# Kernel tuning notes

Measured on AMD Instinct MI355X. Metric: run time of the kernel, lower is better.

Reference implementation:

```python
import jax, jax.numpy as jnp
import numpy as np

B, S, D, H = 2, 2048, 1024, 16
DK = D // H
DFF = 4 * D
EPS = 1e-6


def layer_norm(x, gamma, beta):
    mu = jnp.mean(x, axis=-1, keepdims=True)
    var = jnp.mean(jnp.square(x - mu), axis=-1, keepdims=True)
    return (x - mu) * jax.lax.rsqrt(var + EPS) * gamma + beta


def setup_inputs() -> dict:
    key = jax.random.key(0)
    ks = jax.random.split(key, 10)
    xavier = (6.0 / (D + D)) ** 0.5
    kaiming = (6.0 / D) ** 0.5
    kaiming2 = (6.0 / DFF) ** 0.5
    return {
        "batch_X": jax.random.normal(ks[0], (B, S, D), dtype=jnp.float32),
        "padding_mask": jax.random.randint(ks[1], (B, S), 0, 2, dtype=jnp.int32),
        "W_Q": jax.random.uniform(ks[2], (D, D), jnp.float32, -xavier, xavier),
        "W_K": jax.random.uniform(ks[3], (D, D), jnp.float32, -xavier, xavier),
        "W_V": jax.random.uniform(ks[4], (D, D), jnp.float32, -xavier, xavier),
        "W_O": jax.random.uniform(ks[5], (D, D), jnp.float32, -xavier, xavier),
        "W1": jax.random.uniform(ks[6], (D, DFF), jnp.float32, -kaiming, kaiming),
        "b1": jnp.zeros((DFF,), jnp.float32),
        "W2": jax.random.uniform(ks[7], (DFF, D), jnp.float32, -kaiming2, kaiming2),
        "b2": jnp.zeros((D,), jnp.float32),
        "gamma1": jnp.ones((D,), jnp.float32),
        "beta1": jnp.zeros((D,), jnp.float32),
        "gamma2": jnp.ones((D,), jnp.float32),
        "beta2": jnp.zeros((D,), jnp.float32),
    }


def reference(batch_X, padding_mask, W_Q, W_K, W_V, W_O, W1, b1, W2, b2,
              gamma1, beta1, gamma2, beta2):
    x = batch_X
    b, s, d = x.shape

    # --- multi-head self-attention (use_mask=False: padding mask only) ---
    q = (x @ W_Q).reshape(b, s, H, DK)
    k = (x @ W_K).reshape(b, s, H, DK)
    v = (x @ W_V).reshape(b, s, H, DK)
    scores = jnp.einsum("bqhd,bkhd->bhqk", q, k) / jnp.sqrt(jnp.float32(DK))
    # mask[b,i,j] = (padding_mask[b,i] == 0) for all j: whole query rows are
    # either fully masked (softmax -> NaN -> zeroed in the original) or
    # fully unmasked. Equivalent math: softmax then zero padded query rows.
    probs = jax.nn.softmax(scores, axis=-1)
    keep = (padding_mask != 0).astype(probs.dtype)[:, None, :, None]  # [B,1,S,1]
    probs = probs * keep
    ctx = jnp.einsum("bhqk,bkhd->bqhd", probs, v).reshape(b, s, d)
    attn_out = ctx @ W_O

    # --- residual + LN (dropout identity in eval) ---
    x = x + layer_norm(attn_out, gamma1, beta1)

    # --- FFN ---
    h = jax.nn.relu(x @ W1 + b1)
    ffn_out = h @ W2 + b2
    x = x + layer_norm(ffn_out, gamma2, beta2)
    return x
```

## Files before the change

kernel.cpp:

```cpp
#include <hip/hip_runtime.h>
#include <hip/hip_bf16.h>

#define B 2
#define S 2048
#define D 1024
#define H 16
#define DKh 64
#define DFF 4096
#define M (B*S)

typedef unsigned short u16;
typedef unsigned int u32;
typedef __attribute__((ext_vector_type(8))) short short8;
typedef __attribute__((ext_vector_type(4))) float f32x4;

__device__ __forceinline__ u16 f2bf(float f) {
  union { float f; unsigned u; } v; v.f = f;
  unsigned r = v.u + 0x7fffu + ((v.u >> 16) & 1u);
  return (u16)(r >> 16);
}

__device__ __forceinline__ float bf2f(u16 h) {
  union { u32 u; float f; } v; v.u = ((u32)h) << 16; return v.f;
}

__device__ __forceinline__ u32 pkbf2(float a, float b) {
  __hip_bfloat162 h = __float22bfloat162_rn(make_float2(a, b));
  return *reinterpret_cast<u32*>(&h);
}

__device__ __forceinline__ void gload16(const void* g, void* l) {
  __builtin_amdgcn_global_load_lds((const __attribute__((address_space(1))) void*)g,
                                   (__attribute__((address_space(3))) void*)l, 16, 0, 0);
}

#define SBAR()  __builtin_amdgcn_sched_barrier(0)
#define WBAR()  __builtin_amdgcn_s_barrier()

__device__ __forceinline__ void tcvt_body(const float* __restrict__ W,
    u16* __restrict__ Wt, int K, int N, int n0, int k0, u16 (*l)[65]) {
  const int tx = threadIdx.x & 63, ty = threadIdx.x >> 6;
#pragma unroll
  for (int j = 0; j < 16; ++j) {
    int r = j * 4 + ty;
    l[r][tx] = f2bf(W[(size_t)(k0 + r) * N + n0 + tx]);
  }
  __syncthreads();
#pragma unroll
  for (int j = 0; j < 16; ++j) {
    int r = j * 4 + ty;
    Wt[(size_t)(n0 + r) * K + k0 + tx] = l[tx][r];
  }
}

__global__ __launch_bounds__(256) void prep(const float* __restrict__ X,
    u16* __restrict__ Xb, const float* __restrict__ Wq, const float* __restrict__ Wk,
    const float* __restrict__ Wv, const float* __restrict__ Wo,
    u16* __restrict__ dQKV, u16* __restrict__ dO,
    const float* __restrict__ W1, u16* __restrict__ W1t,
    const float* __restrict__ W2, u16* __restrict__ W2t) {
  __shared__ u16 l[64][65];
  const int bid = blockIdx.x;
  if (bid < 4096) {
    int i = bid * 256 + threadIdx.x;
    float4 v = ((const float4*)X)[i];
    ushort4 o = make_ushort4(f2bf(v.x), f2bf(v.y), f2bf(v.z), f2bf(v.w));
    ((ushort4*)Xb)[i] = o;
  } else if (bid < 5120) {
    int bid2 = bid - 4096;
    int z = bid2 >> 8, r2 = bid2 & 255;
    const float* W = (z == 0) ? Wq : (z == 1) ? Wk : (z == 2) ? Wv : Wo;
    u16* Wt = (z < 3) ? dQKV + (size_t)z * D * D : dO;
    tcvt_body(W, Wt, D, D, (r2 & 15) * 64, (r2 >> 4) * 64, l);
  } else if (bid < 6144) {
    int r2 = bid - 5120;
    tcvt_body(W1, W1t, D, DFF, (r2 & 63) * 64, (r2 >> 6) * 64, l);
  } else {
    int r2 = bid - 6144;
    tcvt_body(W2, W2t, DFF, D, (r2 & 15) * 64, (r2 >> 4) * 64, l);
  }
}

__global__ __launch_bounds__(256) void vtrans(const u16* __restrict__ V,
                                              u16* __restrict__ Vt, int ld) {
  __shared__ u16 l[64][65];
  const int s0 = blockIdx.x * 64, by = blockIdx.y;
  const int b = by >> 4, h = by & 15;
  const int tx = threadIdx.x & 63, ty = threadIdx.x >> 6;
#pragma unroll
  for (int j = 0; j < 16; ++j) {
    int r = j * 4 + ty;
    l[r][tx] = V[(size_t)(b * S + s0 + r) * ld + h * DKh + tx];
  }
  __syncthreads();
#pragma unroll
  for (int j = 0; j < 16; ++j) {
    int r = j * 4 + ty;
    Vt[(size_t)(by * 64 + r) * S + s0 + tx] = l[tx][r];
  }
}

template<int EPI>
__global__ __launch_bounds__(512, 2) void gemm256(const u16* __restrict__ Ag,
    const u16* __restrict__ Bg, void* __restrict__ Cout,
    const float* __restrict__ bias, int Mm, int N, int ld, int Kper,
    int sCols, float qscl) {
  __shared__ u16 lA[2 * 16384];
  __shared__ u16 lB[2 * 16384];
  const int t = threadIdx.x;
  const int lane = t & 63, w = t >> 6;
  const int wm = w >> 2, wn = w & 3;
  const int g = lane >> 4, c = lane & 15;
  const int swz = (c & 7) << 4;

  const int gx = gridDim.x, gy = gridDim.y;
  const int orig = blockIdx.y * gx + blockIdx.x;
  const int qchunk = (gx * gy) >> 3;
  const int wg = (orig & 7) * qchunk + (orig >> 3);
  const int bn0 = (wg % gx) * 256, bm0 = (wg / gx) * 256;
  const int koff = blockIdx.z * Kper;
  const int nk = Kper >> 6;

  f32x4 acc[8][4] = {};
  short8 af[4][2], bf[2][2];

  auto stageA = [&](int h, int buf, int kt) {
#pragma unroll
    for (int i = 0; i < 2; ++i) {
      int chunk = i * 512 + t;
      int rh = chunk >> 3;
      int cb = (chunk & 7) * 16;
      int r = (rh & 63) + (h + 2 * (rh >> 6)) * 64;
      gload16(Ag + (size_t)(bm0 + r) * ld + koff + kt * 64 + ((cb ^ ((r & 7) << 4)) >> 1),
              (void*)((char*)lA + buf * 32768 + h * 16384 + chunk * 16));
    }
  };
  auto stageB = [&](int h, int buf, int kt) {
#pragma unroll
    for (int i = 0; i < 2; ++i) {
      int chunk = i * 512 + t;
      int rh = chunk >> 3;
      int cb = (chunk & 7) * 16;
      int r = (rh & 31) + (h + 2 * (rh >> 5)) * 32;
      gload16(Bg + (size_t)(bn0 + r) * ld + koff + kt * 64 + ((cb ^ ((r & 7) << 4)) >> 1),
              (void*)((char*)lB + buf * 32768 + h * 16384 + chunk * 16));
    }
  };

#define RDA(mh) { const char* lab = (const char*)lA + cur * 32768;                          \
  _Pragma("unroll") for (int mt2 = 0; mt2 < 4; ++mt2)                                       \
    _Pragma("unroll") for (int kc = 0; kc < 2; ++kc)                                        \
      af[mt2][kc] = *(const short8*)(lab + (wm * 64 + (mh) * 128 + mt2 * 16 + c) * 128      \
                                         + ((kc * 64 + g * 16) ^ swz)); }
#define RDB(nh) { const char* lbb = (const char*)lB + cur * 32768;                          \
  _Pragma("unroll") for (int nt2 = 0; nt2 < 2; ++nt2)                                       \
    _Pragma("unroll") for (int kc = 0; kc < 2; ++kc)                                        \
      bf[nt2][kc] = *(const short8*)(lbb + ((nh) * 128 + wn * 32 + nt2 * 16 + c) * 128      \
                                         + ((kc * 64 + g * 16) ^ swz)); }
#define QMFMA(mh, nh) { __builtin_amdgcn_s_setprio(1);                                      \
  _Pragma("unroll") for (int mt2 = 0; mt2 < 4; ++mt2)                                       \
    _Pragma("unroll") for (int nt2 = 0; nt2 < 2; ++nt2)                                     \
      _Pragma("unroll") for (int kc = 0; kc < 2; ++kc)                                      \
        acc[(mh) * 4 + mt2][(nh) * 2 + nt2] = __builtin_amdgcn_mfma_f32_16x16x32_bf16(      \
            af[mt2][kc], bf[nt2][kc], acc[(mh) * 4 + mt2][(nh) * 2 + nt2], 0, 0, 0);        \
  __builtin_amdgcn_s_setprio(0); }

  stageA(0, 0, 0); stageB(0, 0, 0); stageA(1, 0, 0); stageB(1, 0, 0);
  asm volatile("s_waitcnt vmcnt(4)" ::: "memory");
  SBAR(); WBAR(); SBAR();

  int cur = 0;
  for (int kt = 0; kt < nk; ++kt) {
    const bool more = (kt + 1 < nk);
    RDB(0); RDA(0);
    if (more) { stageA(0, cur ^ 1, kt + 1);
                asm volatile("s_waitcnt vmcnt(4)" ::: "memory"); }
    else      { asm volatile("s_waitcnt vmcnt(2)" ::: "memory"); }
    SBAR(); WBAR(); SBAR();
    QMFMA(0, 0);
    SBAR(); WBAR(); SBAR();
    RDA(1);
    if (more) { stageB(0, cur ^ 1, kt + 1);
                asm volatile("s_waitcnt vmcnt(4)" ::: "memory"); }
    else      { asm volatile("s_waitcnt vmcnt(0)" ::: "memory"); }
    SBAR(); WBAR(); SBAR();
    QMFMA(1, 0);
    SBAR(); WBAR(); SBAR();
    RDB(1);
    if (more) stageA(1, cur ^ 1, kt + 1);
    SBAR(); WBAR(); SBAR();
    QMFMA(1, 1);
    SBAR(); WBAR(); SBAR();
    RDA(0);
    if (more) { stageB(1, cur ^ 1, kt + 1);
                asm volatile("s_waitcnt vmcnt(4)" ::: "memory"); }
    SBAR(); WBAR(); SBAR();
    QMFMA(0, 1);
    SBAR(); WBAR(); SBAR();
    cur ^= 1;
  }
#undef RDA
#undef RDB
#undef QMFMA

  float* plane = (EPI == 1) ? ((float*)Cout + (size_t)blockIdx.z * Mm * N) : (float*)Cout;
#pragma unroll
  for (int mt = 0; mt < 8; ++mt) {
#pragma unroll
    for (int nt = 0; nt < 4; ++nt) {
      const int col = bn0 + wn * 64 + nt * 16 + c;
      float bv = (EPI == 2) ? bias[col] : 0.0f;
#pragma unroll
      for (int r = 0; r < 4; ++r) {
        const int row = bm0 + wm * 128 + mt * 16 + g * 4 + r;
        float v = acc[mt][nt][r];
        if (EPI == 2) v = fmaxf(v + bv, 0.0f);
        if (EPI == 0 && col < sCols) v *= qscl;
        if (EPI == 1) plane[(size_t)row * N + col] = v;
        else          ((u16*)Cout)[(size_t)row * N + col] = f2bf(v);
      }
    }
  }
}

__global__ __launch_bounds__(256) void attn_kernel(const u16* __restrict__ Q,
    const u16* __restrict__ Kp, const u16* __restrict__ Vt,
    const int* __restrict__ mask, u16* __restrict__ Ctx, int ldq) {
  __shared__ u16 lK[2][64 * 64];
  __shared__ u16 lV[2][64 * 64];
  __shared__ u16 lP[4 * 4 * 1024];
  const int t = threadIdx.x, lane = t & 63, w = t >> 6;
  const int g = lane >> 4, c = lane & 15;
  const int gx = gridDim.x;
  const int orig = blockIdx.y * gx + blockIdx.x;
  const int qchunk = (gx * gridDim.y) >> 3;
  const int wg = (orig & 7) * qchunk + (orig >> 3);
  const int bx = wg % gx, by = wg / gx;
  const int b = by >> 4, h = by & 15;
  const int q0w = bx * 256 + w * 16;

  short8 qf[4][2];
#pragma unroll
  for (int s = 0; s < 4; ++s)
#pragma unroll
    for (int kc = 0; kc < 2; ++kc)
      qf[s][kc] = *(const short8*)&Q[(size_t)(b * S + q0w + s * 64 + c) * ldq + h * DKh + kc * 32 + g * 8];

  float lsum[4] = {0.f, 0.f, 0.f, 0.f};
  f32x4 accO[4][4] = {};

  auto stage = [&](int buf, int it) {
    const int kv0 = it * 64;
#pragma unroll
    for (int q = 0; q < 2; ++q) {
      int idx = q * 256 + t;
      int row = idx >> 3;
      int colb = (idx & 7) * 16;
      int scol = colb ^ ((row & 7) << 4);
      gload16(Kp + (size_t)(b * S + kv0 + row) * ldq + h * DKh + scol / 2,
              (void*)(&lK[buf][0] + idx * 8));
      gload16(Vt + (size_t)(by * 64 + row) * S + kv0 + scol / 2,
              (void*)(&lV[buf][0] + idx * 8));
    }
  };

  stage(0, 0);
  int cur = 0;
  for (int it = 0; it < S / 64; ++it) {
    __syncthreads();
    if (it + 1 < S / 64) stage(cur ^ 1, it + 1);

#pragma unroll
    for (int ct = 0; ct < 4; ++ct) {
      int row = ct * 16 + c;
      short8 kf0 = *(const short8*)&lK[cur][row * 64 + (((0 * 64 + g * 16) ^ ((row & 7) << 4)) >> 1)];
      short8 kf1 = *(const short8*)&lK[cur][row * 64 + (((1 * 64 + g * 16) ^ ((row & 7) << 4)) >> 1)];
#pragma unroll
      for (int s = 0; s < 4; ++s) {
        f32x4 z = {0.f, 0.f, 0.f, 0.f};
        z = __builtin_amdgcn_mfma_f32_16x16x32_bf16(kf0, qf[s][0], z, 0, 0, 0);
        z = __builtin_amdgcn_mfma_f32_16x16x32_bf16(kf1, qf[s][1], z, 0, 0, 0);
        float p0 = __builtin_amdgcn_exp2f(z[0]);
        float p1 = __builtin_amdgcn_exp2f(z[1]);
        float p2 = __builtin_amdgcn_exp2f(z[2]);
        float p3 = __builtin_amdgcn_exp2f(z[3]);
        lsum[s] += (p0 + p1) + (p2 + p3);
        uint2 pk;
        pk.x = pkbf2(p0, p1);
        pk.y = pkbf2(p2, p3);
        *(uint2*)&lP[(w * 4 + s) * 1024 + c * 64 + (((ct * 32 + g * 8) ^ ((c & 7) << 4)) >> 1)] = pk;
      }
    }

    short8 pa[4][2];
#pragma unroll
    for (int s = 0; s < 4; ++s)
#pragma unroll
      for (int kc = 0; kc < 2; ++kc)
        pa[s][kc] = *(const short8*)&lP[(w * 4 + s) * 1024 + c * 64 + (((kc * 64 + g * 16) ^ ((c & 7) << 4)) >> 1)];

#pragma unroll
    for (int dt = 0; dt < 4; ++dt) {
#pragma unroll
      for (int kc = 0; kc < 2; ++kc) {
        int rowV = dt * 16 + c;
        int bcolV = (kc * 64 + g * 16) ^ ((rowV & 7) << 4);
        short8 vb = *(const short8*)&lV[cur][rowV * 64 + bcolV / 2];
#pragma unroll
        for (int s = 0; s < 4; ++s)
          accO[s][dt] = __builtin_amdgcn_mfma_f32_16x16x32_bf16(pa[s][kc], vb, accO[s][dt], 0, 0, 0);
      }
    }
    cur ^= 1;
  }

#pragma unroll
  for (int s = 0; s < 4; ++s) {
    lsum[s] += __shfl_xor(lsum[s], 16);
    lsum[s] += __shfl_xor(lsum[s], 32);
  }

#pragma unroll
  for (int r = 0; r < 4; ++r) {
    int qrow = g * 4 + r;
#pragma unroll
    for (int s = 0; s < 4; ++s) {
      float lq = __shfl(lsum[s], qrow);
      int q = q0w + s * 64 + qrow;
      float inv = (mask[b * S + q] != 0) ? (1.0f / lq) : 0.0f;
#pragma unroll
      for (int dt = 0; dt < 4; ++dt)
        Ctx[(size_t)(b * S + q) * D + h * DKh + dt * 16 + c] = f2bf(accO[s][dt][r] * inv);
    }
  }
}

__global__ __launch_bounds__(256) void ln_res(const float* __restrict__ planes,
    int np, const float* __restrict__ bias, const float* __restrict__ XresF,
    const u16* __restrict__ XresB, const float* __restrict__ gamma,
    const float* __restrict__ beta, float* __restrict__ outF,
    u16* __restrict__ outB) {
  __shared__ float s1[4], s2[4];
  const int row = blockIdx.x, t = threadIdx.x;
  float4 y = ((const float4*)(planes + (size_t)row * D))[t];
  for (int j = 1; j < np; ++j) {
    const float4 y2 = ((const float4*)(planes + (size_t)j * M * D + (size_t)row * D))[t];
    y.x += y2.x; y.y += y2.y; y.z += y2.z; y.w += y2.w;
  }
  if (bias) {
    const float4 bb = ((const float4*)bias)[t];
    y.x += bb.x; y.y += bb.y; y.z += bb.z; y.w += bb.w;
  }
  float sm = y.x + y.y + y.z + y.w;
  float sq = y.x * y.x + y.y * y.y + y.z * y.z + y.w * y.w;
#pragma unroll
  for (int m2 = 1; m2 <= 32; m2 <<= 1) { sm += __shfl_xor(sm, m2); sq += __shfl_xor(sq, m2); }
  if ((t & 63) == 0) { s1[t >> 6] = sm; s2[t >> 6] = sq; }
  __syncthreads();
  float tot = s1[0] + s1[1] + s1[2] + s1[3];
  float tsq = s2[0] + s2[1] + s2[2] + s2[3];
  float mu = tot * (1.0f / D);
  float var = tsq * (1.0f / D) - mu * mu;
  float rstd = rsqrtf(var + 1e-6f);
  float4 xr;
  if (XresF) {
    xr = ((const float4*)(XresF + (size_t)row * D))[t];
  } else {
    ushort4 xb = ((const ushort4*)(XresB + (size_t)row * D))[t];
    xr.x = bf2f(xb.x); xr.y = bf2f(xb.y); xr.z = bf2f(xb.z); xr.w = bf2f(xb.w);
  }
  const float4 ga = ((const float4*)gamma)[t];
  const float4 be = ((const float4*)beta)[t];
  float4 o;
  o.x = xr.x + (y.x - mu) * rstd * ga.x + be.x;
  o.y = xr.y + (y.y - mu) * rstd * ga.y + be.y;
  o.z = xr.z + (y.z - mu) * rstd * ga.z + be.z;
  o.w = xr.w + (y.w - mu) * rstd * ga.w + be.w;
  if (outF) ((float4*)(outF + (size_t)row * D))[t] = o;
  if (outB) {
    ushort4 ob = make_ushort4(f2bf(o.x), f2bf(o.y), f2bf(o.z), f2bf(o.w));
    ((ushort4*)outB)[(size_t)row * (D / 4) + t] = ob;
  }
}

extern "C" void kernel_launch(void* const* d_in, const int* in_sizes, int n_in,
                              void* d_out, int out_size, void* d_ws, size_t ws_size,
                              hipStream_t stream) {
  const float* X   = (const float*)d_in[0];
  const int*   msk = (const int*)d_in[1];
  const float* WQ  = (const float*)d_in[2];
  const float* WK  = (const float*)d_in[3];
  const float* WV  = (const float*)d_in[4];
  const float* WO  = (const float*)d_in[5];
  const float* W1  = (const float*)d_in[6];
  const float* b1  = (const float*)d_in[7];
  const float* W2  = (const float*)d_in[8];
  const float* b2  = (const float*)d_in[9];
  const float* g1  = (const float*)d_in[10];
  const float* be1 = (const float*)d_in[11];
  const float* g2  = (const float*)d_in[12];
  const float* be2 = (const float*)d_in[13];
  float* out = (float*)d_out;
  const float SCL = 0.18033688011112042f;

  char* ws = (char*)d_ws;
  size_t off = 0;
  auto alloc = [&](size_t bytes) {
    void* p = ws + off;
    off += (bytes + 1023) & ~(size_t)1023;
    return p;
  };
  u16* Xb     = (u16*)alloc((size_t)M * D * 2);
  u16* WQKVt  = (u16*)alloc((size_t)3 * D * D * 2);
  u16* WOt    = (u16*)alloc((size_t)D * D * 2);
  u16* W1t    = (u16*)alloc((size_t)DFF * D * 2);
  u16* W2t    = (u16*)alloc((size_t)D * DFF * 2);
  u16* QKVb   = (u16*)alloc((size_t)M * 3 * D * 2);
  u16* Vt     = (u16*)alloc((size_t)B * H * DKh * S * 2);
  u16* Ctx    = (u16*)alloc((size_t)M * D * 2);
  u16* X1b    = (u16*)alloc((size_t)M * D * 2);
  u16* Hb     = (u16*)alloc((size_t)M * DFF * 2);
  float* PP   = (float*)QKVb;
  if (off > ws_size) return;
  size_t off4 = off;
  float* PP4 = (float*)(ws + off4);
  off4 += (size_t)4 * M * D * 4;
  const bool split4 = (off4 <= ws_size);

  dim3 blk(256), blk5(512);

  prep<<<dim3(7168), blk, 0, stream>>>(X, Xb, WQ, WK, WV, WO, WQKVt, WOt, W1, W1t, W2, W2t);
  gemm256<0><<<dim3(3 * D / 256, M / 256), blk5, 0, stream>>>(Xb, WQKVt, QKVb, nullptr, M, 3 * D, D, D, D, SCL);
  vtrans<<<dim3(S / 64, B * H), blk, 0, stream>>>(QKVb + 2 * D, Vt, 3 * D);
  attn_kernel<<<dim3(S / 256, B * H), blk, 0, stream>>>(QKVb, QKVb + D, Vt, msk, Ctx, 3 * D);
  gemm256<1><<<dim3(D / 256, M / 256, 2), blk5, 0, stream>>>(Ctx, WOt, PP, nullptr, M, D, D, D / 2, 0, 1.0f);
  ln_res<<<dim3(M), blk, 0, stream>>>(PP, 2, nullptr, X, nullptr, g1, be1, nullptr, X1b);
  gemm256<2><<<dim3(DFF / 256, M / 256), blk5, 0, stream>>>(X1b, W1t, Hb, b1, M, DFF, D, D, 0, 1.0f);
  if (split4) {
    gemm256<1><<<dim3(D / 256, M / 256, 4), blk5, 0, stream>>>(Hb, W2t, PP4, nullptr, M, D, DFF, DFF / 4, 0, 1.0f);
    ln_res<<<dim3(M), blk, 0, stream>>>(PP4, 4, b2, nullptr, X1b, g2, be2, out, nullptr);
  } else {
    gemm256<1><<<dim3(D / 256, M / 256, 2), blk5, 0, stream>>>(Hb, W2t, PP, nullptr, M, D, DFF, DFF / 2, 0, 1.0f);
    ln_res<<<dim3(M), blk, 0, stream>>>(PP, 2, b2, nullptr, X1b, g2, be2, out, nullptr);
  }
}
```

Baseline: 252.2 us.

## Rewrite attention with 32x32 MFMA and register-resident P via permlane swaps

Switches the attention kernel from 16x16x32 MFMA tiles to 32x32x16 tiles, with each wave owning 32 query rows. The exponentiated scores are packed to bf16 and moved into the A-operand layout with v_permlane32_swap, which removes the LDS round trip for P and its shared buffer. The grid doubles because each block now covers 128 queries instead of 256, so K/V tiles are reused across fewer queries per block. This lowers LDS traffic and register pressure in exchange for more K/V global loads, and relies on the gfx950 permlane instruction layout being correct.

```diff
diff --git a/kernel.cpp b/kernel.cpp
--- a/kernel.cpp
+++ b/kernel.cpp
@@ -13,6 +13,8 @@
 typedef unsigned int u32;
 typedef __attribute__((ext_vector_type(8))) short short8;
 typedef __attribute__((ext_vector_type(4))) float f32x4;
+typedef __attribute__((ext_vector_type(16))) float f32x16;
+typedef __attribute__((ext_vector_type(4))) unsigned u32x4;
 
 __device__ __forceinline__ u16 f2bf(float f) {
   union { float f; unsigned u; } v; v.f = f;
@@ -228,26 +230,23 @@
     const int* __restrict__ mask, u16* __restrict__ Ctx, int ldq) {
   __shared__ u16 lK[2][64 * 64];
   __shared__ u16 lV[2][64 * 64];
-  __shared__ u16 lP[4 * 4 * 1024];
   const int t = threadIdx.x, lane = t & 63, w = t >> 6;
-  const int g = lane >> 4, c = lane & 15;
+  const int l31 = lane & 31, hi = lane >> 5;
   const int gx = gridDim.x;
   const int orig = blockIdx.y * gx + blockIdx.x;
   const int qchunk = (gx * gridDim.y) >> 3;
   const int wg = (orig & 7) * qchunk + (orig >> 3);
   const int bx = wg % gx, by = wg / gx;
   const int b = by >> 4, h = by & 15;
-  const int q0w = bx * 256 + w * 16;
-
-  short8 qf[4][2];
+  const int q0 = bx * 128 + w * 32;
+
+  short8 qreg[4];
 #pragma unroll
   for (int s = 0; s < 4; ++s)
-#pragma unroll
-    for (int kc = 0; kc < 2; ++kc)
-      qf[s][kc] = *(const short8*)&Q[(size_t)(b * S + q0w + s * 64 + c) * ldq + h * DKh + kc * 32 + g * 8];
-
-  float lsum[4] = {0.f, 0.f, 0.f, 0.f};
-  f32x4 accO[4][4] = {};
+    qreg[s] = *(const short8*)&Q[(size_t)(b * S + q0 + l31) * ldq + h * DKh + s * 16 + hi * 8];
+
+  float lsum = 0.0f;
+  f32x16 accO[2] = {};
 
   auto stage = [&](int buf, int it) {
     const int kv0 = it * 64;
@@ -270,68 +269,61 @@
     __syncthreads();
     if (it + 1 < S / 64) stage(cur ^ 1, it + 1);
 
-#pragma unroll
-    for (int ct = 0; ct < 4; ++ct) {
-      int row = ct * 16 + c;
-      short8 kf0 = *(const short8*)&lK[cur][row * 64 + (((0 * 64 + g * 16) ^ ((row & 7) << 4)) >> 1)];
-      short8 kf1 = *(const short8*)&lK[cur][row * 64 + (((1 * 64 + g * 16) ^ ((row & 7) << 4)) >> 1)];
+    short8 pa[4];
+#pragma unroll
+    for (int kvb = 0; kvb < 2; ++kvb) {
+      f32x16 z = {0.f,0.f,0.f,0.f,0.f,0.f,0.f,0.f,0.f,0.f,0.f,0.f,0.f,0.f,0.f,0.f};
 #pragma unroll
       for (int s = 0; s < 4; ++s) {
-        f32x4 z = {0.f, 0.f, 0.f, 0.f};
-        z = __builtin_amdgcn_mfma_f32_16x16x32_bf16(kf0, qf[s][0], z, 0, 0, 0);
-        z = __builtin_amdgcn_mfma_f32_16x16x32_bf16(kf1, qf[s][1], z, 0, 0, 0);
-        float p0 = __builtin_amdgcn_exp2f(z[0]);
-        float p1 = __builtin_amdgcn_exp2f(z[1]);
-        float p2 = __builtin_amdgcn_exp2f(z[2]);
-        float p3 = __builtin_amdgcn_exp2f(z[3]);
-        lsum[s] += (p0 + p1) + (p2 + p3);
-        uint2 pk;
-        pk.x = pkbf2(p0, p1);
-        pk.y = pkbf2(p2, p3);
-        *(uint2*)&lP[(w * 4 + s) * 1024 + c * 64 + (((ct * 32 + g * 8) ^ ((c & 7) << 4)) >> 1)] = pk;
+        int row = kvb * 32 + l31;
+        int bcol = (s * 32 + hi * 16) ^ ((row & 7) << 4);
+        short8 kf = *(const short8*)&lK[cur][row * 64 + bcol / 2];
+        z = __builtin_amdgcn_mfma_f32_32x32x16_bf16(kf, qreg[s], z, 0, 0, 0);
       }
-    }
-
-    short8 pa[4][2];
-#pragma unroll
-    for (int s = 0; s < 4; ++s)
-#pragma unroll
-      for (int kc = 0; kc < 2; ++kc)
-        pa[s][kc] = *(const short8*)&lP[(w * 4 + s) * 1024 + c * 64 + (((kc * 64 + g * 16) ^ ((c & 7) << 4)) >> 1)];
-
-#pragma unroll
-    for (int dt = 0; dt < 4; ++dt) {
-#pragma unroll
-      for (int kc = 0; kc < 2; ++kc) {
-        int rowV = dt * 16 + c;
-        int bcolV = (kc * 64 + g * 16) ^ ((rowV & 7) << 4);
-        short8 vb = *(const short8*)&lV[cur][rowV * 64 + bcolV / 2];
-#pragma unroll
-        for (int s = 0; s < 4; ++s)
-          accO[s][dt] = __builtin_amdgcn_mfma_f32_16x16x32_bf16(pa[s][kc], vb, accO[s][dt], 0, 0, 0);
+      float p[16];
+#pragma unroll
+      for (int i2 = 0; i2 < 16; ++i2) {
+        p[i2] = __builtin_amdgcn_exp2f(z[i2]);
+        lsum += p[i2];
       }
+      u32 x0 = pkbf2(p[0],  p[1]),  y0 = pkbf2(p[4],  p[5]);
+      u32 x1 = pkbf2(p[2],  p[3]),  y1 = pkbf2(p[6],  p[7]);
+      asm("v_permlane32_swap_b32 %0, %1" : "+v"(x0), "+v"(y0));
+      asm("v_permlane32_swap_b32 %0, %1" : "+v"(x1), "+v"(y1));
+      u32 x2 = pkbf2(p[8],  p[9]),  y2 = pkbf2(p[12], p[13]);
+      u32 x3 = pkbf2(p[10], p[11]), y3 = pkbf2(p[14], p[15]);
+      asm("v_permlane32_swap_b32 %0, %1" : "+v"(x2), "+v"(y2));
+      asm("v_permlane32_swap_b32 %0, %1" : "+v"(x3), "+v"(y3));
+      u32x4 w0 = {x0, x1, y0, y1};
+      u32x4 w1 = {x2, x3, y2, y3};
+      pa[kvb * 2 + 0] = *reinterpret_cast<short8*>(&w0);
+      pa[kvb * 2 + 1] = *reinterpret_cast<short8*>(&w1);
+    }
+
+#pragma unroll
+    for (int ks = 0; ks < 4; ++ks) {
+#pragma unroll
+      for (int nb = 0; nb < 2; ++nb) {
+        int row = nb * 32 + l31;
+        int bcol = (ks * 32 + hi * 16) ^ ((row & 7) << 4);
+        short8 vf = *(const short8*)&lV[cur][row * 64 + bcol / 2];
+        accO[nb] = __builtin_amdgcn_mfma_f32_32x32x16_bf16(pa[ks], vf, accO[nb], 0, 0, 0);
+      }
     }
     cur ^= 1;
   }
 
-#pragma unroll
-  for (int s = 0; s < 4; ++s) {
-    lsum[s] += __shfl_xor(lsum[s], 16);
-    lsum[s] += __shfl_xor(lsum[s], 32);
-  }
-
-#pragma unroll
-  for (int r = 0; r < 4; ++r) {
-    int qrow = g * 4 + r;
-#pragma unroll
-    for (int s = 0; s < 4; ++s) {
-      float lq = __shfl(lsum[s], qrow);
-      int q = q0w + s * 64 + qrow;
-      float inv = (mask[b * S + q] != 0) ? (1.0f / lq) : 0.0f;
-#pragma unroll
-      for (int dt = 0; dt < 4; ++dt)
-        Ctx[(size_t)(b * S + q) * D + h * DKh + dt * 16 + c] = f2bf(accO[s][dt][r] * inv);
-    }
+  lsum += __shfl_xor(lsum, 32);
+
+  const int* mrow = mask + b * S + q0;
+#pragma unroll
+  for (int reg = 0; reg < 16; ++reg) {
+    const int qr = (reg & 3) + 8 * (reg >> 2) + 4 * hi;
+    float lq = __shfl(lsum, qr);
+    float inv = (mrow[qr] != 0) ? (1.0f / lq) : 0.0f;
+    const size_t base = (size_t)(b * S + q0 + qr) * D + h * DKh;
+    Ctx[base + 0 * 32 + l31] = f2bf(accO[0][reg] * inv);
+    Ctx[base + 1 * 32 + l31] = f2bf(accO[1][reg] * inv);
   }
 }
 
@@ -432,7 +424,7 @@
   prep<<<dim3(7168), blk, 0, stream>>>(X, Xb, WQ, WK, WV, WO, WQKVt, WOt, W1, W1t, W2, W2t);
   gemm256<0><<<dim3(3 * D / 256, M / 256), blk5, 0, stream>>>(Xb, WQKVt, QKVb, nullptr, M, 3 * D, D, D, D, SCL);
   vtrans<<<dim3(S / 64, B * H), blk, 0, stream>>>(QKVb + 2 * D, Vt, 3 * D);
-  attn_kernel<<<dim3(S / 256, B * H), blk, 0, stream>>>(QKVb, QKVb + D, Vt, msk, Ctx, 3 * D);
+  attn_kernel<<<dim3(S / 128, B * H), blk, 0, stream>>>(QKVb, QKVb + D, Vt, msk, Ctx, 3 * D);
   gemm256<1><<<dim3(D / 256, M / 256, 2), blk5, 0, stream>>>(Ctx, WOt, PP, nullptr, M, D, D, D / 2, 0, 1.0f);
   ln_res<<<dim3(M), blk, 0, stream>>>(PP, 2, nullptr, X, nullptr, g1, be1, nullptr, X1b);
   gemm256<2><<<dim3(DFF / 256, M / 256), blk5, 0, stream>>>(X1b, W1t, Hb, b1, M, DFF, D, D, 0, 1.0f);
```

Result: faster. 241.9 us (-4.1%).
